# Kernel tuning notes

Hardware: AMD Instinct MI355X
Metric: run time of the kernel (lower is better)

Reference implementation:

```python
import jax, jax.numpy as jnp
import numpy as np

N = 100000   # nodes
E = 1000000  # edges
D = 128      # input_dim
H = 128      # hidden_dim
P = 128      # proj_dim


def setup_inputs() -> dict:
    key = jax.random.key(0)
    ks = jax.random.split(key, 12)
    def lin(k, fi, fo):
        return jax.random.normal(k, (fi, fo), jnp.float32) / np.sqrt(fi).astype(np.float32)
    x = jax.random.normal(ks[0], (N, D), jnp.float32)
    edge_index = jax.random.randint(ks[1], (2, E), 0, N, dtype=jnp.int32)
    return {
        "x": x,
        "edge_index": edge_index,
        "W1": lin(ks[2], D, H), "b1": jnp.zeros((H,), jnp.float32),
        "W2": lin(ks[3], H, H), "b2": jnp.zeros((H,), jnp.float32),
        "Wp1": lin(ks[4], H, P), "bp1": jnp.zeros((P,), jnp.float32),
        "prelu_a": jnp.float32(0.25),
        "Wp2": lin(ks[5], P, P), "bp2": jnp.zeros((P,), jnp.float32),
    }


def _gcn_conv(h, W, b, src, dst):
    # PyG GCNConv: h' = D^{-1/2} (A + I) D^{-1/2} (h W) + b
    h = h @ W                                   # [N, H]
    loop = jnp.arange(N, dtype=src.dtype)
    s = jnp.concatenate([src, loop])            # add self-loops
    d = jnp.concatenate([dst, loop])
    deg = jax.ops.segment_sum(jnp.ones(s.shape, h.dtype), d, num_segments=N)
    dinv = jax.lax.rsqrt(jnp.maximum(deg, 1.0))  # deg >= 1 due to self-loops
    norm = dinv[s] * dinv[d]                     # [E+N]
    msg = h[s] * norm[:, None]                   # gather + scale
    return jax.ops.segment_sum(msg, d, num_segments=N) + b


def reference(x, edge_index, W1, b1, W2, b2, Wp1, bp1, prelu_a, Wp2, bp2):
    src, dst = edge_index[0], edge_index[1]
    z = jax.nn.relu(_gcn_conv(x, W1, b1, src, dst))   # dropout p=0 -> identity
    z = jax.nn.relu(_gcn_conv(z, W2, b2, src, dst))
    h = z @ Wp1 + bp1
    h = jnp.where(h > 0, h, prelu_a * h)              # PReLU
    p = h @ Wp2 + bp2
    return (z, p)
```

## Files before the change

### kernel.cpp

```cpp
#include <hip/hip_runtime.h>

typedef __bf16 bf16x8 __attribute__((ext_vector_type(8)));
typedef float  f32x4  __attribute__((ext_vector_type(4)));
typedef unsigned short us8 __attribute__((ext_vector_type(8)));
typedef unsigned short us4 __attribute__((ext_vector_type(4)));

__device__ __forceinline__ float bf2f(unsigned short u) {
    return __builtin_bit_cast(float, (unsigned int)u << 16);
}
__device__ __forceinline__ unsigned short f2bf(float f) {
    return __builtin_bit_cast(unsigned short, (__bf16)f);
}

__global__ void prep_w4(const float* __restrict__ W0, const float* __restrict__ W1,
                        const float* __restrict__ W2, const float* __restrict__ W3,
                        unsigned short* __restrict__ wt) {
    int i = blockIdx.x * 256 + threadIdx.x;
    int m = i >> 14, r = i & 16383;
    const float* W = (m == 0) ? W0 : (m == 1) ? W1 : (m == 2) ? W2 : W3;
    float f = W[r];
    int k = r >> 7, n = r & 127;
    __bf16 h = (__bf16)f;
    __bf16 l = (__bf16)(f - (float)h);
    unsigned short* base = wt + m * 32768;
    base[n * 128 + k]         = __builtin_bit_cast(unsigned short, h);
    base[16384 + n * 128 + k] = __builtin_bit_cast(unsigned short, l);
}

__global__ void to_bf16(const float* __restrict__ in, unsigned short* __restrict__ out, int n4) {
    int i = blockIdx.x * 256 + threadIdx.x;
    if (i < n4) {
        f32x4 v = ((const f32x4*)in)[i];
        us4 o;
        o[0] = f2bf(v[0]); o[1] = f2bf(v[1]); o[2] = f2bf(v[2]); o[3] = f2bf(v[3]);
        ((us4*)out)[i] = o;
    }
}

__global__ void count_deg(const int* __restrict__ dst, int* __restrict__ cnt, int E) {
    int e = blockIdx.x * 256 + threadIdx.x;
    if (e < E) atomicAdd(&cnt[dst[e]], 1);
}

__global__ void scanA(const int* __restrict__ cnt, int* __restrict__ rowptr,
                      int* __restrict__ bsum, int N) {
    __shared__ int s[1024];
    int t = threadIdx.x;
    int idx = blockIdx.x * 1024 + t;
    int v = (idx < N) ? cnt[idx] : 0;
    int sum = v;
    s[t] = sum;
    __syncthreads();
    for (int o = 1; o < 1024; o <<= 1) {
        int u = (t >= o) ? s[t - o] : 0;
        __syncthreads();
        sum += u;
        s[t] = sum;
        __syncthreads();
    }
    if (idx < N) rowptr[idx] = sum - v;
    if (t == 1023) bsum[blockIdx.x] = sum;
}

__global__ void scanB(int* __restrict__ bsum, int nb) {
    __shared__ int s[128];
    int t = threadIdx.x;
    int v = (t < nb) ? bsum[t] : 0;
    int sum = v;
    s[t] = sum;
    __syncthreads();
    for (int o = 1; o < 128; o <<= 1) {
        int u = (t >= o) ? s[t - o] : 0;
        __syncthreads();
        sum += u;
        s[t] = sum;
        __syncthreads();
    }
    if (t < nb) bsum[t] = sum - v;
}

__global__ void scanC(int* __restrict__ rowptr, const int* __restrict__ bsum,
                      int* __restrict__ cnt_cursor, float* __restrict__ dinv,
                      float* __restrict__ selfw, int N, int E) {
    int i = blockIdx.x * 256 + threadIdx.x;
    if (i < N) {
        int c = cnt_cursor[i];
        int a = rowptr[i] + bsum[i >> 10];
        rowptr[i] = a;
        cnt_cursor[i] = a;
        float dv = rsqrtf((float)(c + 1));
        dinv[i] = dv;
        selfw[i] = dv * dv;
    }
    if (i == 0) rowptr[N] = E;
}

__global__ void fill_csr(const int* __restrict__ src, const int* __restrict__ dst,
                         int* __restrict__ cursor, const float* __restrict__ dinv,
                         int2* __restrict__ epack, int E) {
    int e = blockIdx.x * 256 + threadIdx.x;
    if (e < E) {
        int s = src[e];
        int d = dst[e];
        float w = dinv[s] * dinv[d];
        int p = atomicAdd(&cursor[d], 1);
        int2 rec;
        rec.x = s;
        rec.y = __builtin_bit_cast(int, w);
        epack[p] = rec;
    }
}

__global__ __launch_bounds__(256) void gemm128s(
    const unsigned short* __restrict__ Ahi, const unsigned short* __restrict__ WhiT,
    const unsigned short* __restrict__ WloT, const float* __restrict__ bias,
    const float* __restrict__ prelu_a, float* __restrict__ Cf,
    unsigned short* __restrict__ Cb, int M, int mode)
{
    __shared__ unsigned short sHi[128 * 136];
    __shared__ unsigned short sLo[128 * 136];
    const int tid = threadIdx.x;

    for (int i = tid; i < 2048; i += 256) {
        int row = i >> 4, seg = i & 15;
        *(us8*)(&sHi[row * 136 + seg * 8]) = *(const us8*)(WhiT + row * 128 + seg * 8);
        *(us8*)(&sLo[row * 136 + seg * 8]) = *(const us8*)(WloT + row * 128 + seg * 8);
    }
    __syncthreads();

    const int lane = tid & 63;
    const int wave = tid >> 6;
    const int lc   = lane & 15;
    const int quad = lane >> 4;
    const int rowBlock = blockIdx.x * 128 + wave * 32;

    f32x4 acc[2][8];
    const f32x4 z4 = {0.f, 0.f, 0.f, 0.f};
#pragma unroll
    for (int rs = 0; rs < 2; ++rs)
#pragma unroll
        for (int t = 0; t < 8; ++t) acc[rs][t] = z4;

#pragma unroll
    for (int ks = 0; ks < 4; ++ks) {
        const int kf = ks * 32 + quad * 8;
        bf16x8 a[2];
#pragma unroll
        for (int rs = 0; rs < 2; ++rs) {
            int r = rowBlock + rs * 16 + lc;
            if (r > M - 1) r = M - 1;
            a[rs] = __builtin_bit_cast(bf16x8, *(const us8*)(Ahi + (size_t)r * 128 + kf));
        }
#pragma unroll
        for (int t = 0; t < 8; ++t) {
            bf16x8 bhi = __builtin_bit_cast(bf16x8, *(const us8*)(&sHi[(t * 16 + lc) * 136 + kf]));
            bf16x8 blo = __builtin_bit_cast(bf16x8, *(const us8*)(&sLo[(t * 16 + lc) * 136 + kf]));
#pragma unroll
            for (int rs = 0; rs < 2; ++rs) {
                acc[rs][t] = __builtin_amdgcn_mfma_f32_16x16x32_bf16(a[rs], bhi, acc[rs][t], 0, 0, 0);
                acc[rs][t] = __builtin_amdgcn_mfma_f32_16x16x32_bf16(a[rs], blo, acc[rs][t], 0, 0, 0);
            }
        }
    }

    float av = (mode == 1) ? prelu_a[0] : 0.f;
#pragma unroll
    for (int t = 0; t < 8; ++t) {
        int gcol = t * 16 + lc;
        float bv = (mode != 0) ? bias[gcol] : 0.f;
#pragma unroll
        for (int rs = 0; rs < 2; ++rs) {
#pragma unroll
            for (int i = 0; i < 4; ++i) {
                int r = rowBlock + rs * 16 + quad * 4 + i;
                if (r < M) {
                    float v = acc[rs][t][i] + bv;
                    if (mode == 1) v = (v > 0.f) ? v : av * v;
                    if (mode == 2) Cf[(size_t)r * 128 + gcol] = v;
                    else           Cb[(size_t)r * 128 + gcol] = f2bf(v);
                }
            }
        }
    }
}

__global__ __launch_bounds__(256) void aggregate(
    const unsigned short* __restrict__ Hhi, const float* __restrict__ selfw,
    const int* __restrict__ rowptr, const int2* __restrict__ epack,
    const float* __restrict__ bias, float* __restrict__ outF,
    unsigned short* __restrict__ outHi, int N)
{
    const int tid = threadIdx.x;
    const int g = tid >> 5;
    const int l = tid & 31;
    const int n = blockIdx.x * 8 + g;
    if (n >= N) return;

    const int beg = rowptr[n], end = rowptr[n + 1];
    const size_t fo = (size_t)l * 4;

    f32x4 a0 = {0.f, 0.f, 0.f, 0.f};
    f32x4 a1 = a0, a2 = a0, a3 = a0;

    int i = beg;
    for (; i + 3 < end; i += 4) {
        int2 e0 = epack[i];
        int2 e1 = epack[i + 1];
        int2 e2 = epack[i + 2];
        int2 e3 = epack[i + 3];
        us4 h0 = *(const us4*)(Hhi + (size_t)e0.x * 128 + fo);
        us4 h1 = *(const us4*)(Hhi + (size_t)e1.x * 128 + fo);
        us4 h2 = *(const us4*)(Hhi + (size_t)e2.x * 128 + fo);
        us4 h3 = *(const us4*)(Hhi + (size_t)e3.x * 128 + fo);
        float w0 = __builtin_bit_cast(float, e0.y);
        float w1 = __builtin_bit_cast(float, e1.y);
        float w2 = __builtin_bit_cast(float, e2.y);
        float w3 = __builtin_bit_cast(float, e3.y);
#pragma unroll
        for (int j = 0; j < 4; ++j) a0[j] += w0 * bf2f(h0[j]);
#pragma unroll
        for (int j = 0; j < 4; ++j) a1[j] += w1 * bf2f(h1[j]);
#pragma unroll
        for (int j = 0; j < 4; ++j) a2[j] += w2 * bf2f(h2[j]);
#pragma unroll
        for (int j = 0; j < 4; ++j) a3[j] += w3 * bf2f(h3[j]);
    }
    for (; i < end; ++i) {
        int2 e0 = epack[i];
        us4 h0 = *(const us4*)(Hhi + (size_t)e0.x * 128 + fo);
        float w0 = __builtin_bit_cast(float, e0.y);
#pragma unroll
        for (int j = 0; j < 4; ++j) a0[j] += w0 * bf2f(h0[j]);
    }

    float sw = selfw[n];
    us4 sh = *(const us4*)(Hhi + (size_t)n * 128 + fo);
    f32x4 b4 = *(const f32x4*)(bias + l * 4);
    f32x4 sum = (a0 + a1) + (a2 + a3);
    f32x4 v;
    us4 ob;
#pragma unroll
    for (int j = 0; j < 4; ++j) {
        v[j] = fmaxf(sum[j] + sw * bf2f(sh[j]) + b4[j], 0.f);
        ob[j] = f2bf(v[j]);
    }
    if (outF) *(f32x4*)(outF + (size_t)n * 128 + fo) = v;
    *(us4*)(outHi + (size_t)n * 128 + fo) = ob;
}

extern "C" void kernel_launch(void* const* d_in, const int* in_sizes, int n_in,
                              void* d_out, int out_size, void* d_ws, size_t ws_size,
                              hipStream_t stream)
{
    const float* x   = (const float*)d_in[0];
    const int*   ei  = (const int*)d_in[1];
    const float* W1  = (const float*)d_in[2];
    const float* b1  = (const float*)d_in[3];
    const float* W2  = (const float*)d_in[4];
    const float* b2  = (const float*)d_in[5];
    const float* Wp1 = (const float*)d_in[6];
    const float* bp1 = (const float*)d_in[7];
    const float* pa  = (const float*)d_in[8];
    const float* Wp2 = (const float*)d_in[9];
    const float* bp2 = (const float*)d_in[10];

    const int N = in_sizes[0] / 128;
    const int E = in_sizes[1] / 2;
    const int* src = ei;
    const int* dst = ei + E;

    float* outF = (float*)d_out;
    float* zbuf = outF;
    float* pbuf = outF + (size_t)N * 128;

    char* w = (char*)d_ws;
    size_t off = 0;
    auto alloc = [&](size_t bytes) {
        void* p = w + off;
        off = (off + bytes + 255) & ~(size_t)255;
        return p;
    };
    unsigned short* S1 = (unsigned short*)alloc((size_t)N * 128 * sizeof(unsigned short));
    unsigned short* S2 = (unsigned short*)alloc((size_t)N * 128 * sizeof(unsigned short));
    float* dinv   = (float*)alloc((size_t)N * sizeof(float));
    float* selfw  = (float*)alloc((size_t)N * sizeof(float));
    int*   rowptr = (int*)alloc((size_t)(N + 1) * sizeof(int));
    int*   cntcur = (int*)alloc((size_t)N * sizeof(int));
    int2*  epack  = (int2*)alloc((size_t)E * sizeof(int2));
    int*   bsum   = (int*)alloc(1024);
    unsigned short* wt = (unsigned short*)alloc((size_t)4 * 2 * 128 * 128 * sizeof(unsigned short));
    (void)ws_size; (void)n_in; (void)out_size;

    auto hiP = [&](int m) { return wt + (size_t)m * 32768; };
    auto loP = [&](int m) { return wt + (size_t)m * 32768 + 16384; };

    hipLaunchKernelGGL(prep_w4, dim3(256), dim3(256), 0, stream, W1, W2, Wp1, Wp2, wt);
    const int n4 = N * 128 / 4;
    hipLaunchKernelGGL(to_bf16, dim3((n4 + 255) / 256), dim3(256), 0, stream, x, S1, n4);

    hipMemsetAsync(cntcur, 0, (size_t)N * sizeof(int), stream);
    const int nb = (N + 1023) >> 10;
    hipLaunchKernelGGL(count_deg, dim3((E + 255) / 256), dim3(256), 0, stream, dst, cntcur, E);
    hipLaunchKernelGGL(scanA,     dim3(nb), dim3(1024), 0, stream, cntcur, rowptr, bsum, N);
    hipLaunchKernelGGL(scanB,     dim3(1), dim3(128), 0, stream, bsum, nb);
    hipLaunchKernelGGL(scanC,     dim3((N + 255) / 256), dim3(256), 0, stream, rowptr, bsum, cntcur, dinv, selfw, N, E);
    hipLaunchKernelGGL(fill_csr,  dim3((E + 255) / 256), dim3(256), 0, stream, src, dst, cntcur, dinv, epack, E);

    const int gb = (N + 127) / 128;
    const int ab = (N + 7) / 8;
    hipLaunchKernelGGL(gemm128s, dim3(gb), dim3(256), 0, stream, S1, hiP(0), loP(0),
                       (const float*)nullptr, (const float*)nullptr, (float*)nullptr, S2, N, 0);
    hipLaunchKernelGGL(aggregate, dim3(ab), dim3(256), 0, stream, S2, selfw, rowptr, epack,
                       b1, (float*)nullptr, S1, N);
    hipLaunchKernelGGL(gemm128s, dim3(gb), dim3(256), 0, stream, S1, hiP(1), loP(1),
                       (const float*)nullptr, (const float*)nullptr, (float*)nullptr, S2, N, 0);
    hipLaunchKernelGGL(aggregate, dim3(ab), dim3(256), 0, stream, S2, selfw, rowptr, epack,
                       b2, zbuf, S1, N);
    hipLaunchKernelGGL(gemm128s, dim3(gb), dim3(256), 0, stream, S1, hiP(2), loP(2),
                       bp1, pa, (float*)nullptr, S2, N, 1);
    hipLaunchKernelGGL(gemm128s, dim3(gb), dim3(256), 0, stream, S2, hiP(3), loP(3),
                       bp2, (const float*)nullptr, pbuf, (unsigned short*)nullptr, N, 2);
}
```

Measured before the change: 493.0 us.

## Fuse CSR build into persistent grid-barrier kernel, fold casts and projections

Result: slower. 712.6 us (+44.5%).

```diff
diff --git a/kernel.cpp b/kernel.cpp
--- a/kernel.cpp
+++ b/kernel.cpp
@@ -12,109 +12,120 @@
     return __builtin_bit_cast(unsigned short, (__bf16)f);
 }
 
-__global__ void prep_w4(const float* __restrict__ W0, const float* __restrict__ W1,
-                        const float* __restrict__ W2, const float* __restrict__ W3,
-                        unsigned short* __restrict__ wt) {
-    int i = blockIdx.x * 256 + threadIdx.x;
-    int m = i >> 14, r = i & 16383;
-    const float* W = (m == 0) ? W0 : (m == 1) ? W1 : (m == 2) ? W2 : W3;
-    float f = W[r];
-    int k = r >> 7, n = r & 127;
-    __bf16 h = (__bf16)f;
-    __bf16 l = (__bf16)(f - (float)h);
-    unsigned short* base = wt + m * 32768;
-    base[n * 128 + k]         = __builtin_bit_cast(unsigned short, h);
-    base[16384 + n * 128 + k] = __builtin_bit_cast(unsigned short, l);
-}
-
-__global__ void to_bf16(const float* __restrict__ in, unsigned short* __restrict__ out, int n4) {
-    int i = blockIdx.x * 256 + threadIdx.x;
-    if (i < n4) {
-        f32x4 v = ((const f32x4*)in)[i];
-        us4 o;
-        o[0] = f2bf(v[0]); o[1] = f2bf(v[1]); o[2] = f2bf(v[2]); o[3] = f2bf(v[3]);
-        ((us4*)out)[i] = o;
-    }
-}
-
-__global__ void count_deg(const int* __restrict__ dst, int* __restrict__ cnt, int E) {
-    int e = blockIdx.x * 256 + threadIdx.x;
-    if (e < E) atomicAdd(&cnt[dst[e]], 1);
-}
-
-__global__ void scanA(const int* __restrict__ cnt, int* __restrict__ rowptr,
-                      int* __restrict__ bsum, int N) {
-    __shared__ int s[1024];
-    int t = threadIdx.x;
-    int idx = blockIdx.x * 1024 + t;
-    int v = (idx < N) ? cnt[idx] : 0;
-    int sum = v;
-    s[t] = sum;
-    __syncthreads();
-    for (int o = 1; o < 1024; o <<= 1) {
-        int u = (t >= o) ? s[t - o] : 0;
+#define MEGA_NB 448
+
+__device__ __forceinline__ void gridbar(int* bar, int k) {
+    __syncthreads();
+    if (threadIdx.x == 0) {
+        __threadfence();
+        __hip_atomic_fetch_add(bar, 1, __ATOMIC_RELAXED, __HIP_MEMORY_SCOPE_AGENT);
+        while (__hip_atomic_load(bar, __ATOMIC_RELAXED, __HIP_MEMORY_SCOPE_AGENT) < MEGA_NB * k)
+            __builtin_amdgcn_s_sleep(2);
+        __threadfence();
+    }
+    __syncthreads();
+}
+
+__global__ __launch_bounds__(256, 2) void csr_mega(
+    const float* __restrict__ W0, const float* __restrict__ W1f,
+    const float* __restrict__ W2f, const float* __restrict__ W3f,
+    unsigned short* __restrict__ wt,
+    const int* __restrict__ src, const int* __restrict__ dst,
+    int* __restrict__ cnt, int* __restrict__ rowptr, int* __restrict__ csum,
+    float* __restrict__ dinv, float* __restrict__ selfw, int* __restrict__ cursor,
+    int2* __restrict__ epack, int* __restrict__ bar, int N, int E)
+{
+    const int tid = threadIdx.x;
+    const int gtid = blockIdx.x * 256 + tid;
+    const int GT = MEGA_NB * 256;
+    __shared__ int s[256];
+    __shared__ int carry_s;
+
+    if (gtid < 65536) {
+        int m = gtid >> 14, r = gtid & 16383;
+        const float* W = (m == 0) ? W0 : (m == 1) ? W1f : (m == 2) ? W2f : W3f;
+        float f = W[r];
+        int k = r >> 7, n = r & 127;
+        __bf16 h = (__bf16)f;
+        __bf16 l = (__bf16)(f - (float)h);
+        unsigned short* base = wt + m * 32768;
+        base[n * 128 + k]         = __builtin_bit_cast(unsigned short, h);
+        base[16384 + n * 128 + k] = __builtin_bit_cast(unsigned short, l);
+    }
+    for (int e = gtid; e < E; e += GT) atomicAdd(&cnt[dst[e]], 1);
+    gridbar(bar, 1);
+
+    const int nchunks = (N + 255) >> 8;
+    for (int c = blockIdx.x; c < nchunks; c += MEGA_NB) {
+        int idx = c * 256 + tid;
+        int v = (idx < N) ? cnt[idx] : 0;
+        int sum = v;
+        s[tid] = sum;
         __syncthreads();
-        sum += u;
-        s[t] = sum;
+        for (int o = 1; o < 256; o <<= 1) {
+            int u = (tid >= o) ? s[tid - o] : 0;
+            __syncthreads();
+            sum += u;
+            s[tid] = sum;
+            __syncthreads();
+        }
+        if (idx < N) rowptr[idx] = sum - v;
+        if (tid == 255) csum[c] = sum;
         __syncthreads();
     }
-    if (idx < N) rowptr[idx] = sum - v;
-    if (t == 1023) bsum[blockIdx.x] = sum;
-}
-
-__global__ void scanB(int* __restrict__ bsum, int nb) {
-    __shared__ int s[128];
-    int t = threadIdx.x;
-    int v = (t < nb) ? bsum[t] : 0;
-    int sum = v;
-    s[t] = sum;
-    __syncthreads();
-    for (int o = 1; o < 128; o <<= 1) {
-        int u = (t >= o) ? s[t - o] : 0;
+    gridbar(bar, 2);
+
+    if (blockIdx.x == 0) {
+        if (tid == 0) carry_s = 0;
         __syncthreads();
-        sum += u;
-        s[t] = sum;
-        __syncthreads();
-    }
-    if (t < nb) bsum[t] = sum - v;
-}
-
-__global__ void scanC(int* __restrict__ rowptr, const int* __restrict__ bsum,
-                      int* __restrict__ cnt_cursor, float* __restrict__ dinv,
-                      float* __restrict__ selfw, int N, int E) {
-    int i = blockIdx.x * 256 + threadIdx.x;
-    if (i < N) {
-        int c = cnt_cursor[i];
-        int a = rowptr[i] + bsum[i >> 10];
+        for (int base = 0; base < nchunks; base += 256) {
+            int idx = base + tid;
+            int v = (idx < nchunks) ? csum[idx] : 0;
+            int sum = v;
+            s[tid] = sum;
+            __syncthreads();
+            for (int o = 1; o < 256; o <<= 1) {
+                int u = (tid >= o) ? s[tid - o] : 0;
+                __syncthreads();
+                sum += u;
+                s[tid] = sum;
+                __syncthreads();
+            }
+            int c0 = carry_s;
+            if (idx < nchunks) csum[idx] = c0 + sum - v;
+            __syncthreads();
+            if (tid == 255) carry_s = c0 + sum;
+            __syncthreads();
+        }
+    }
+    gridbar(bar, 3);
+
+    for (int i = gtid; i < N; i += GT) {
+        int a = rowptr[i] + csum[i >> 8];
         rowptr[i] = a;
-        cnt_cursor[i] = a;
-        float dv = rsqrtf((float)(c + 1));
+        cursor[i] = a;
+        float dv = rsqrtf((float)(cnt[i] + 1));
         dinv[i] = dv;
         selfw[i] = dv * dv;
     }
-    if (i == 0) rowptr[N] = E;
-}
-
-__global__ void fill_csr(const int* __restrict__ src, const int* __restrict__ dst,
-                         int* __restrict__ cursor, const float* __restrict__ dinv,
-                         int2* __restrict__ epack, int E) {
-    int e = blockIdx.x * 256 + threadIdx.x;
-    if (e < E) {
-        int s = src[e];
-        int d = dst[e];
-        float w = dinv[s] * dinv[d];
+    if (gtid == 0) rowptr[N] = E;
+    gridbar(bar, 4);
+
+    for (int e = gtid; e < E; e += GT) {
+        int sv = src[e], d = dst[e];
+        float w = dinv[sv] * dinv[d];
         int p = atomicAdd(&cursor[d], 1);
         int2 rec;
-        rec.x = s;
+        rec.x = sv;
         rec.y = __builtin_bit_cast(int, w);
         epack[p] = rec;
     }
 }
 
 __global__ __launch_bounds__(256) void gemm128s(
-    const unsigned short* __restrict__ Ahi, const unsigned short* __restrict__ WhiT,
-    const unsigned short* __restrict__ WloT, const float* __restrict__ bias,
-    const float* __restrict__ prelu_a, float* __restrict__ Cf,
+    const void* __restrict__ A, int aF32,
+    const unsigned short* __restrict__ WhiT, const unsigned short* __restrict__ WloT,
+    const float* __restrict__ bias, float* __restrict__ Cf,
     unsigned short* __restrict__ Cb, int M, int mode)
 {
     __shared__ unsigned short sHi[128 * 136];
@@ -149,7 +160,19 @@
         for (int rs = 0; rs < 2; ++rs) {
             int r = rowBlock + rs * 16 + lc;
             if (r > M - 1) r = M - 1;
-            a[rs] = __builtin_bit_cast(bf16x8, *(const us8*)(Ahi + (size_t)r * 128 + kf));
+            if (aF32) {
+                const f32x4* ap = (const f32x4*)((const float*)A + (size_t)r * 128 + kf);
+                f32x4 a0 = ap[0], a1 = ap[1];
+                bf16x8 av;
+#pragma unroll
+                for (int j = 0; j < 4; ++j) av[j] = (__bf16)a0[j];
+#pragma unroll
+                for (int j = 0; j < 4; ++j) av[4 + j] = (__bf16)a1[j];
+                a[rs] = av;
+            } else {
+                a[rs] = __builtin_bit_cast(bf16x8,
+                        *(const us8*)((const unsigned short*)A + (size_t)r * 128 + kf));
+            }
         }
 #pragma unroll
         for (int t = 0; t < 8; ++t) {
@@ -163,7 +186,6 @@
         }
     }
 
-    float av = (mode == 1) ? prelu_a[0] : 0.f;
 #pragma unroll
     for (int t = 0; t < 8; ++t) {
         int gcol = t * 16 + lc;
@@ -175,10 +197,131 @@
                 int r = rowBlock + rs * 16 + quad * 4 + i;
                 if (r < M) {
                     float v = acc[rs][t][i] + bv;
-                    if (mode == 1) v = (v > 0.f) ? v : av * v;
                     if (mode == 2) Cf[(size_t)r * 128 + gcol] = v;
                     else           Cb[(size_t)r * 128 + gcol] = f2bf(v);
                 }
+            }
+        }
+    }
+}
+
+__global__ __launch_bounds__(256) void proj2(
+    const unsigned short* __restrict__ Z, const unsigned short* __restrict__ wtp1,
+    const unsigned short* __restrict__ wtp2, const float* __restrict__ bp1,
+    const float* __restrict__ prelu_a, const float* __restrict__ bp2,
+    unsigned short* __restrict__ T1, float* __restrict__ P, int M)
+{
+    __shared__ unsigned short sHi[128 * 136];
+    __shared__ unsigned short sLo[128 * 136];
+    const int tid = threadIdx.x;
+    const int lane = tid & 63;
+    const int wave = tid >> 6;
+    const int lc   = lane & 15;
+    const int quad = lane >> 4;
+    const int rowBlock = blockIdx.x * 128 + wave * 32;
+    const f32x4 z4 = {0.f, 0.f, 0.f, 0.f};
+
+    for (int i = tid; i < 2048; i += 256) {
+        int row = i >> 4, seg = i & 15;
+        *(us8*)(&sHi[row * 136 + seg * 8]) = *(const us8*)(wtp1 + row * 128 + seg * 8);
+        *(us8*)(&sLo[row * 136 + seg * 8]) = *(const us8*)(wtp1 + 16384 + row * 128 + seg * 8);
+    }
+    __syncthreads();
+
+    f32x4 acc[2][8];
+#pragma unroll
+    for (int rs = 0; rs < 2; ++rs)
+#pragma unroll
+        for (int t = 0; t < 8; ++t) acc[rs][t] = z4;
+
+#pragma unroll
+    for (int ks = 0; ks < 4; ++ks) {
+        const int kf = ks * 32 + quad * 8;
+        bf16x8 a[2];
+#pragma unroll
+        for (int rs = 0; rs < 2; ++rs) {
+            int r = rowBlock + rs * 16 + lc;
+            if (r > M - 1) r = M - 1;
+            a[rs] = __builtin_bit_cast(bf16x8, *(const us8*)(Z + (size_t)r * 128 + kf));
+        }
+#pragma unroll
+        for (int t = 0; t < 8; ++t) {
+            bf16x8 bhi = __builtin_bit_cast(bf16x8, *(const us8*)(&sHi[(t * 16 + lc) * 136 + kf]));
+            bf16x8 blo = __builtin_bit_cast(bf16x8, *(const us8*)(&sLo[(t * 16 + lc) * 136 + kf]));
+#pragma unroll
+            for (int rs = 0; rs < 2; ++rs) {
+                acc[rs][t] = __builtin_amdgcn_mfma_f32_16x16x32_bf16(a[rs], bhi, acc[rs][t], 0, 0, 0);
+                acc[rs][t] = __builtin_amdgcn_mfma_f32_16x16x32_bf16(a[rs], blo, acc[rs][t], 0, 0, 0);
+            }
+        }
+    }
+
+    float av = prelu_a[0];
+#pragma unroll
+    for (int t = 0; t < 8; ++t) {
+        int gcol = t * 16 + lc;
+        float bv = bp1[gcol];
+#pragma unroll
+        for (int rs = 0; rs < 2; ++rs) {
+#pragma unroll
+            for (int i = 0; i < 4; ++i) {
+                int r = rowBlock + rs * 16 + quad * 4 + i;
+                if (r < M) {
+                    float v = acc[rs][t][i] + bv;
+                    v = (v > 0.f) ? v : av * v;
+                    T1[(size_t)r * 128 + gcol] = f2bf(v);
+                }
+            }
+        }
+    }
+
+    __threadfence();
+    __syncthreads();
+
+    for (int i = tid; i < 2048; i += 256) {
+        int row = i >> 4, seg = i & 15;
+        *(us8*)(&sHi[row * 136 + seg * 8]) = *(const us8*)(wtp2 + row * 128 + seg * 8);
+        *(us8*)(&sLo[row * 136 + seg * 8]) = *(const us8*)(wtp2 + 16384 + row * 128 + seg * 8);
+    }
+    __syncthreads();
+
+#pragma unroll
+    for (int rs = 0; rs < 2; ++rs)
+#pragma unroll
+        for (int t = 0; t < 8; ++t) acc[rs][t] = z4;
+
+#pragma unroll
+    for (int ks = 0; ks < 4; ++ks) {
+        const int kf = ks * 32 + quad * 8;
+        bf16x8 a[2];
+#pragma unroll
+        for (int rs = 0; rs < 2; ++rs) {
+            int r = rowBlock + rs * 16 + lc;
+            if (r > M - 1) r = M - 1;
+            a[rs] = __builtin_bit_cast(bf16x8, *(const us8*)(T1 + (size_t)r * 128 + kf));
+        }
+#pragma unroll
+        for (int t = 0; t < 8; ++t) {
+            bf16x8 bhi = __builtin_bit_cast(bf16x8, *(const us8*)(&sHi[(t * 16 + lc) * 136 + kf]));
+            bf16x8 blo = __builtin_bit_cast(bf16x8, *(const us8*)(&sLo[(t * 16 + lc) * 136 + kf]));
+#pragma unroll
+            for (int rs = 0; rs < 2; ++rs) {
+                acc[rs][t] = __builtin_amdgcn_mfma_f32_16x16x32_bf16(a[rs], bhi, acc[rs][t], 0, 0, 0);
+                acc[rs][t] = __builtin_amdgcn_mfma_f32_16x16x32_bf16(a[rs], blo, acc[rs][t], 0, 0, 0);
+            }
+        }
+    }
+
+#pragma unroll
+    for (int t = 0; t < 8; ++t) {
+        int gcol = t * 16 + lc;
+        float bv = bp2[gcol];
+#pragma unroll
+        for (int rs = 0; rs < 2; ++rs) {
+#pragma unroll
+            for (int i = 0; i < 4; ++i) {
+                int r = rowBlock + rs * 16 + quad * 4 + i;
+                if (r < M) P[(size_t)r * 128 + gcol] = acc[rs][t][i] + bv;
             }
         }
     }
@@ -199,44 +342,53 @@
     const int beg = rowptr[n], end = rowptr[n + 1];
     const size_t fo = (size_t)l * 4;
 
-    f32x4 a0 = {0.f, 0.f, 0.f, 0.f};
-    f32x4 a1 = a0, a2 = a0, a3 = a0;
+    f32x4 acc[4];
+    const f32x4 z4 = {0.f, 0.f, 0.f, 0.f};
+#pragma unroll
+    for (int u = 0; u < 4; ++u) acc[u] = z4;
 
     int i = beg;
-    for (; i + 3 < end; i += 4) {
-        int2 e0 = epack[i];
-        int2 e1 = epack[i + 1];
-        int2 e2 = epack[i + 2];
-        int2 e3 = epack[i + 3];
-        us4 h0 = *(const us4*)(Hhi + (size_t)e0.x * 128 + fo);
-        us4 h1 = *(const us4*)(Hhi + (size_t)e1.x * 128 + fo);
-        us4 h2 = *(const us4*)(Hhi + (size_t)e2.x * 128 + fo);
-        us4 h3 = *(const us4*)(Hhi + (size_t)e3.x * 128 + fo);
-        float w0 = __builtin_bit_cast(float, e0.y);
-        float w1 = __builtin_bit_cast(float, e1.y);
-        float w2 = __builtin_bit_cast(float, e2.y);
-        float w3 = __builtin_bit_cast(float, e3.y);
-#pragma unroll
-        for (int j = 0; j < 4; ++j) a0[j] += w0 * bf2f(h0[j]);
-#pragma unroll
-        for (int j = 0; j < 4; ++j) a1[j] += w1 * bf2f(h1[j]);
-#pragma unroll
-        for (int j = 0; j < 4; ++j) a2[j] += w2 * bf2f(h2[j]);
-#pragma unroll
-        for (int j = 0; j < 4; ++j) a3[j] += w3 * bf2f(h3[j]);
+    for (; i + 7 < end; i += 8) {
+        int2 e[8];
+        us4 h[8];
+#pragma unroll
+        for (int u = 0; u < 8; ++u) e[u] = epack[i + u];
+#pragma unroll
+        for (int u = 0; u < 8; ++u) h[u] = *(const us4*)(Hhi + (size_t)e[u].x * 128 + fo);
+#pragma unroll
+        for (int u = 0; u < 8; ++u) {
+            float w = __builtin_bit_cast(float, e[u].y);
+#pragma unroll
+            for (int j = 0; j < 4; ++j) acc[u & 3][j] += w * bf2f(h[u][j]);
+        }
+    }
+    if (i + 3 < end) {
+        int2 e[4];
+        us4 h[4];
+#pragma unroll
+        for (int u = 0; u < 4; ++u) e[u] = epack[i + u];
+#pragma unroll
+        for (int u = 0; u < 4; ++u) h[u] = *(const us4*)(Hhi + (size_t)e[u].x * 128 + fo);
+#pragma unroll
+        for (int u = 0; u < 4; ++u) {
+            float w = __builtin_bit_cast(float, e[u].y);
+#pragma unroll
+            for (int j = 0; j < 4; ++j) acc[u][j] += w * bf2f(h[u][j]);
+        }
+        i += 4;
     }
     for (; i < end; ++i) {
         int2 e0 = epack[i];
         us4 h0 = *(const us4*)(Hhi + (size_t)e0.x * 128 + fo);
         float w0 = __builtin_bit_cast(float, e0.y);
 #pragma unroll
-        for (int j = 0; j < 4; ++j) a0[j] += w0 * bf2f(h0[j]);
+        for (int j = 0; j < 4; ++j) acc[0][j] += w0 * bf2f(h0[j]);
     }
 
     float sw = selfw[n];
     us4 sh = *(const us4*)(Hhi + (size_t)n * 128 + fo);
     f32x4 b4 = *(const f32x4*)(bias + l * 4);
-    f32x4 sum = (a0 + a1) + (a2 + a3);
+    f32x4 sum = (acc[0] + acc[1]) + (acc[2] + acc[3]);
     f32x4 v;
     us4 ob;
 #pragma unroll
@@ -285,39 +437,33 @@
     float* dinv   = (float*)alloc((size_t)N * sizeof(float));
     float* selfw  = (float*)alloc((size_t)N * sizeof(float));
     int*   rowptr = (int*)alloc((size_t)(N + 1) * sizeof(int));
-    int*   cntcur = (int*)alloc((size_t)N * sizeof(int));
+    int*   cnt    = (int*)alloc((size_t)(N + 8) * sizeof(int));
+    int*   bar    = cnt + N;
+    int*   cursor = (int*)alloc((size_t)N * sizeof(int));
+    int*   csum   = (int*)alloc((size_t)1024 * sizeof(int));
     int2*  epack  = (int2*)alloc((size_t)E * sizeof(int2));
-    int*   bsum   = (int*)alloc(1024);
     unsigned short* wt = (unsigned short*)alloc((size_t)4 * 2 * 128 * 128 * sizeof(unsigned short));
     (void)ws_size; (void)n_in; (void)out_size;
 
     auto hiP = [&](int m) { return wt + (size_t)m * 32768; };
     auto loP = [&](int m) { return wt + (size_t)m * 32768 + 16384; };
 
-    hipLaunchKernelGGL(prep_w4, dim3(256), dim3(256), 0, stream, W1, W2, Wp1, Wp2, wt);
-    const int n4 = N * 128 / 4;
-    hipLaunchKernelGGL(to_bf16, dim3((n4 + 255) / 256), dim3(256), 0, stream, x, S1, n4);
-
-    hipMemsetAsync(cntcur, 0, (size_t)N * sizeof(int), stream);
-    const int nb = (N + 1023) >> 10;
-    hipLaunchKernelGGL(count_deg, dim3((E + 255) / 256), dim3(256), 0, stream, dst, cntcur, E);
-    hipLaunchKernelGGL(scanA,     dim3(nb), dim3(1024), 0, stream, cntcur, rowptr, bsum, N);
-    hipLaunchKernelGGL(scanB,     dim3(1), dim3(128), 0, stream, bsum, nb);
-    hipLaunchKernelGGL(scanC,     dim3((N + 255) / 256), dim3(256), 0, stream, rowptr, bsum, cntcur, dinv, selfw, N, E);
-    hipLaunchKernelGGL(fill_csr,  dim3((E + 255) / 256), dim3(256), 0, stream, src, dst, cntcur, dinv, epack, E);
+    hipMemsetAsync(cnt, 0, (size_t)(N + 8) * sizeof(int), stream);
+
+    hipLaunchKernelGGL(csr_mega, dim3(MEGA_NB), dim3(256), 0, stream,
+                       W1, W2, Wp1, Wp2, wt, src, dst, cnt, rowptr, csum,
+                       dinv, selfw, cursor, epack, bar, N, E);
 
     const int gb = (N + 127) / 128;
     const int ab = (N + 7) / 8;
-    hipLaunchKernelGGL(gemm128s, dim3(gb), dim3(256), 0, stream, S1, hiP(0), loP(0),
-                       (const float*)nullptr, (const float*)nullptr, (float*)nullptr, S2, N, 0);
+    hipLaunchKernelGGL(gemm128s, dim3(gb), dim3(256), 0, stream, (const void*)x, 1,
+                       hiP(0), loP(0), (const float*)nullptr, (float*)nullptr, S2, N, 0);
     hipLaunchKernelGGL(aggregate, dim3(ab), dim3(256), 0, stream, S2, selfw, rowptr, epack,
                        b1, (float*)nullptr, S1, N);
-    hipLaunchKernelGGL(gemm128s, dim3(gb), dim3(256), 0, stream, S1, hiP(1), loP(1),
-                       (const float*)nullptr, (const float*)nullptr, (float*)nullptr, S2, N, 0);
+    hipLaunchKernelGGL(gemm128s, dim3(gb), dim3(256), 0, stream, (const void*)S1, 0,
+                       hiP(1), loP(1), (const float*)nullptr, (float*)nullptr, S2, N, 0);
     hipLaunchKernelGGL(aggregate, dim3(ab), dim3(256), 0, stream, S2, selfw, rowptr, epack,
                        b2, zbuf, S1, N);
-    hipLaunchKernelGGL(gemm128s, dim3(gb), dim3(256), 0, stream, S1, hiP(2), loP(2),
-                       bp1, pa, (float*)nullptr, S2, N, 1);
-    hipLaunchKernelGGL(gemm128s, dim3(gb), dim3(256), 0, stream, S2, hiP(3), loP(3),
-                       bp2, (const float*)nullptr, pbuf, (unsigned short*)nullptr, N, 2);
-}
+    hipLaunchKernelGGL(proj2, dim3(gb), dim3(256), 0, stream, S1, hiP(2), hiP(3),
+                       bp1, pa, bp2, S2, pbuf, N);
+}
```
